# Kernel optimization log

Measured on AMD Instinct MI355X. Metric: run time of the kernel, lower is better.

## Reference

```python
import jax, jax.numpy as jnp
import numpy as np

N = 128          # seed length cfg.n
EXTRA_RANDOM = 1 # cfg.extra_random_masks


def _make_masks(n: int, extra: int) -> np.ndarray:
    i = np.arange(n, dtype=np.int64)
    # Thue-Morse: parity of popcount(i)
    tm = np.array([bin(v).count('1') & 1 for v in i], dtype=np.uint8)
    # Sierpinski: row (n-1) of Pascal's triangle mod 2 (Lucas' theorem)
    sp = (((n - 1) & i) == i).astype(np.uint8)
    masks = [sp, tm]
    rng = np.random.default_rng(1234)
    for _ in range(extra):
        masks.append(rng.integers(0, 2, size=n, dtype=np.uint8))
    return np.stack(masks, axis=0)  # (K, n)


def setup_inputs() -> dict:
    key = jax.random.key(0)
    ks = jax.random.split(key, 8)
    B, n = 64, N
    T = n * (n + 1) // 2  # 8256
    H = 1024
    x = jax.random.randint(ks[0], (B, n), 0, 2, dtype=jnp.int32)
    masks = jnp.asarray(_make_masks(n, EXTRA_RANDOM))
    def lin(k, fan_in, fan_out):
        lim = 1.0 / np.sqrt(fan_in)
        return jax.random.uniform(k, (fan_in, fan_out), jnp.float32, -lim, lim)
    W0 = lin(ks[1], T, H); b0 = jnp.zeros((H,), jnp.float32)
    W1 = lin(ks[2], H, H); b1 = jnp.zeros((H,), jnp.float32)
    Wo = lin(ks[3], H, 1); bo = jnp.zeros((1,), jnp.float32)
    return {"x": x, "masks": masks, "W0": W0, "b0": b0,
            "W1": W1, "b1": b1, "Wo": Wo, "bo": bo}


def _features(x, masks):
    # x: (B, n) ints in {0,1}; masks: (K, n) uint8
    xb = x.astype(jnp.uint8)
    B, n = xb.shape
    # L3: dihedral orbit = n rotations + n rotations of the reversal -> 2n seeds
    idx = (jnp.arange(n)[:, None] + jnp.arange(n)[None, :]) % n  # (n, n)
    rot = xb[:, idx]                # (B, n, n)
    rev = xb[:, ::-1][:, idx]       # (B, n, n)
    seeds = jnp.concatenate([rot, rev], axis=1)  # (B, 2n, n)
    # L4: keep each seed plus XOR with each mask -> (1+K) variants per seed
    masked = jnp.bitwise_xor(seeds[:, :, None, :], masks[None, None, :, :])  # (B,2n,K,n)
    all_seeds = jnp.concatenate([seeds[:, :, None, :], masked], axis=2)
    M = all_seeds.shape[1] * all_seeds.shape[2]
    all_seeds = all_seeds.reshape(B, M, n)  # (B, M, n) uint8
    # XNOR triangle: row0 = seed, row_{k+1}[j] = xnor(row_k[j], row_k[j+1])
    rows = [all_seeds]
    cur = all_seeds
    for _ in range(n - 1):
        cur = 1 - jnp.bitwise_xor(cur[..., :-1], cur[..., 1:])
        rows.append(cur)
    feats = jnp.concatenate(rows, axis=-1)          # (B, M, T(n)) uint8
    f = jnp.mean(feats, axis=1, dtype=jnp.float32)  # mean pool over transforms
    return 2.0 * f - 1.0                            # {0,1} -> {-1,+1}


def reference(x, masks, W0, b0, W1, b1, Wo, bo):
    f = _features(x, masks)
    h = jax.nn.relu(f @ W0 + b0)
    h = jax.nn.relu(h @ W1 + b1)
    return h @ Wo + bo  # (B, 1) logits
```

## Files before the change

### kernel.cpp

```cpp
#include <hip/hip_runtime.h>
#include <cstdint>

#define DEVFN __device__ __forceinline__

struct U128 { unsigned long long lo, hi; };

DEVFN U128 rotr128(U128 w, int s) {
    U128 r;
    if (s == 64) { r.lo = w.hi; r.hi = w.lo; return r; }
    if (s < 64) {
        r.lo = (w.lo >> s) | (w.hi << (64 - s));
        r.hi = (w.hi >> s) | (w.lo << (64 - s));
    } else {
        int t = s - 64;
        unsigned long long lo = w.hi, hi = w.lo;
        r.lo = (lo >> t) | (hi << (64 - t));
        r.hi = (hi >> t) | (lo << (64 - t));
    }
    return r;
}

DEVFN U128 shr128(U128 w, int s) {
    U128 r;
    if (s == 64) { r.lo = w.hi; r.hi = 0ull; return r; }
    if (s < 64) {
        r.lo = (w.lo >> s) | (w.hi << (64 - s));
        r.hi = w.hi >> s;
    } else {
        r.lo = w.hi >> (s - 64); r.hi = 0ull;
    }
    return r;
}

__global__ __launch_bounds__(256) void kB(const int* __restrict__ x,
                                          const int* __restrict__ masks,
                                          const float* __restrict__ W0,
                                          float* __restrict__ S,
                                          float* __restrict__ A2,
                                          float* __restrict__ G2) {
    int bid = blockIdx.x;
    int tid = threadIdx.x;

    if (bid == 768) {
        int b = tid >> 2;
        int rc = tid & 3;
        const int* xb = x + b * 128;
        U128 w; w.lo = 0ull; w.hi = 0ull;
        #pragma unroll
        for (int p = 0; p < 64; ++p) w.lo |= (unsigned long long)(xb[p] & 1) << p;
        #pragma unroll
        for (int p = 0; p < 64; ++p) w.hi |= (unsigned long long)(xb[64 + p] & 1) << p;
        int r0 = rc * 32;
        if (r0 & 32) { U128 t = rotr128(w, 32); w.lo ^= t.lo; w.hi ^= t.hi; }
        if (r0 & 64) { U128 t = rotr128(w, 64); w.lo ^= t.lo; w.hi ^= t.hi; }
        for (int rr = 0; rr < 32; ++rr) {
            int r = r0 + rr;
            int pc = __popcll(w.lo) + __popcll(w.hi);
            int sv = (r == 0) ? pc : (128 - pc);
            S[b * 128 + r] = (float)(2 * sv);
            U128 t = rotr128(w, 1);
            w.lo ^= t.lo; w.hi ^= t.hi;
        }
        return;
    }

    int hc = bid & 3;
    int y  = bid >> 2;
    int r, jstart, jend, slice;
    if (y < 128) { r = y >> 1; slice = y & 1; jstart = slice * 64; jend = (slice == 0) ? 64 : (128 - r); }
    else         { r = y - 64;  slice = 0;    jstart = 0;          jend = 128 - r; }
    int L = jend - jstart;

    int lane = tid & 63;
    int g    = tid >> 6;

    __shared__ unsigned long long mw[3][2];
    __shared__ float cA[64], cG[64];
    __shared__ float4 partA[4][64];
    __shared__ float4 partG[4][64];

    if (tid < 128) {
        int half = tid >> 6;
        int lane_ = tid & 63;
        #pragma unroll
        for (int k = 0; k < 3; ++k) {
            unsigned long long bal = __ballot(masks[k * 128 + half * 64 + lane_] & 1);
            if (lane_ == 0) mw[k][half] = bal;
        }
    }
    __syncthreads();
    if (tid < 64) {
        int j = jstart + tid;
        int c = 0;
        #pragma unroll
        for (int k = 0; k < 3; ++k) {
            U128 m; m.lo = mw[k][0]; m.hi = mw[k][1];
            #pragma unroll
            for (int s = 1; s <= 64; s <<= 1) {
                if (r & s) { U128 t = shr128(m, s); m.lo ^= t.lo; m.hi ^= t.hi; }
            }
            int bit = (j < 64) ? (int)((m.lo >> j) & 1) : (int)((m.hi >> (j - 64)) & 1);
            c += bit;
        }
        cA[tid] = 0.5f * (float)c - 1.0f;
        cG[tid] = (float)(2 - c) * (1.0f / 256.0f);
    }
    __syncthreads();

    int off = r * 128 - (r * (r - 1)) / 2;
    const float* base = W0 + (size_t)(off + jstart) * 1024 + hc * 256 + lane * 4;
    float4 aA = {0.f, 0.f, 0.f, 0.f}, aG = {0.f, 0.f, 0.f, 0.f};
    #pragma unroll 4
    for (int jj = g; jj < L; jj += 4) {
        float4 v = *(const float4*)(base + (size_t)jj * 1024);
        float ca = cA[jj], cg = cG[jj];
        aA.x += ca * v.x; aA.y += ca * v.y; aA.z += ca * v.z; aA.w += ca * v.w;
        aG.x += cg * v.x; aG.y += cg * v.y; aG.z += cg * v.z; aG.w += cg * v.w;
    }
    partA[g][lane] = aA;
    partG[g][lane] = aG;
    __syncthreads();

    if (tid < 64) {
        float4 sA = partA[0][tid], sG = partG[0][tid];
        #pragma unroll
        for (int gg = 1; gg < 4; ++gg) {
            float4 pA = partA[gg][tid], pG = partG[gg][tid];
            sA.x += pA.x; sA.y += pA.y; sA.z += pA.z; sA.w += pA.w;
            sG.x += pG.x; sG.y += pG.y; sG.z += pG.z; sG.w += pG.w;
        }
        int row = slice * 128 + r;
        *(float4*)(A2 + (size_t)row * 1024 + hc * 256 + tid * 4) = sA;
        *(float4*)(G2 + (size_t)row * 1024 + hc * 256 + tid * 4) = sG;
    }
}

__global__ __launch_bounds__(256) void kF(const float* __restrict__ A2,
                                          const float* __restrict__ G2,
                                          const float* __restrict__ S,
                                          const float* __restrict__ b0,
                                          const float* __restrict__ W1,
                                          float* __restrict__ z1part) {
    int hc = blockIdx.x;
    int kc = blockIdx.y;
    int bs = blockIdx.z;
    int tid = threadIdx.x;

    __shared__ float W1sh[64][128];
    __shared__ float Ssh[16][128];
    __shared__ float h0sh[16][64];

    #pragma unroll
    for (int t = 0; t < 32; ++t) {
        int idx = tid + t * 256;
        int kk = idx >> 7, hcl = idx & 127;
        W1sh[kk][hcl] = W1[(kc * 64 + kk) * 1024 + hc * 128 + hcl];
    }
    #pragma unroll
    for (int t = 0; t < 8; ++t) {
        int idx = tid + t * 256;
        int bl = idx >> 7, r = idx & 127;
        Ssh[bl][r] = S[(bs * 16 + bl) * 128 + r];
    }
    __syncthreads();

    {
        int k = tid & 63;
        int bg = tid >> 6;
        const float* a2p = A2 + kc * 64 + k;
        const float* g2p = G2 + kc * 64 + k;
        float accA = 0.f;
        float acc[4] = {0.f, 0.f, 0.f, 0.f};
        #pragma unroll 8
        for (int row = 0; row < 192; ++row) {
            float a = a2p[row * 1024];
            float g = g2p[row * 1024];
            accA += a;
            int r = row & 127;
            #pragma unroll
            for (int bb = 0; bb < 4; ++bb)
                acc[bb] += Ssh[bg * 4 + bb][r] * g;
        }
        float base = b0[kc * 64 + k] + accA;
        #pragma unroll
        for (int bb = 0; bb < 4; ++bb)
            h0sh[bg * 4 + bb][k] = fmaxf(base + acc[bb], 0.f);
    }
    __syncthreads();

    {
        int hcol = tid & 127;
        int bg2 = tid >> 7;
        float acc2[8];
        #pragma unroll
        for (int i = 0; i < 8; ++i) acc2[i] = 0.f;
        #pragma unroll 4
        for (int kk = 0; kk < 64; ++kk) {
            float w = W1sh[kk][hcol];
            #pragma unroll
            for (int bb = 0; bb < 8; ++bb)
                acc2[bb] += h0sh[bg2 * 8 + bb][kk] * w;
        }
        #pragma unroll
        for (int bb = 0; bb < 8; ++bb) {
            int b = bs * 16 + bg2 * 8 + bb;
            z1part[(kc * 64 + b) * 1024 + hc * 128 + hcol] = acc2[bb];
        }
    }
}

__global__ __launch_bounds__(1024) void kE(const float* __restrict__ z1part,
                                           const float* __restrict__ b1,
                                           const float* __restrict__ Wo,
                                           const float* __restrict__ bo,
                                           float* __restrict__ out) {
    int b = blockIdx.x;
    int h = threadIdx.x;
    float z = b1[h];
    #pragma unroll
    for (int kc = 0; kc < 16; ++kc) z += z1part[(kc * 64 + b) * 1024 + h];
    float acc = fmaxf(z, 0.f) * Wo[h];
    #pragma unroll
    for (int off = 32; off >= 1; off >>= 1) acc += __shfl_down(acc, off);
    __shared__ float red[16];
    if ((h & 63) == 0) red[h >> 6] = acc;
    __syncthreads();
    if (h == 0) {
        float s = bo[0];
        #pragma unroll
        for (int i = 0; i < 16; ++i) s += red[i];
        out[b] = s;
    }
}

extern "C" void kernel_launch(void* const* d_in, const int* in_sizes, int n_in,
                              void* d_out, int out_size, void* d_ws, size_t ws_size,
                              hipStream_t stream) {
    const int*   x     = (const int*)d_in[0];
    const int*   masks = (const int*)d_in[1];
    const float* W0    = (const float*)d_in[2];
    const float* b0    = (const float*)d_in[3];
    const float* W1    = (const float*)d_in[4];
    const float* b1    = (const float*)d_in[5];
    const float* Wo    = (const float*)d_in[6];
    const float* bo    = (const float*)d_in[7];
    float* out = (float*)d_out;

    char* ws = (char*)d_ws;
    float* S      = (float*)(ws);
    float* A2     = (float*)(ws + (32u   << 10));
    float* G2     = (float*)(ws + (800u  << 10));
    float* z1part = (float*)(ws + (1568u << 10));

    kB<<<769, 256, 0, stream>>>(x, masks, W0, S, A2, G2);
    kF<<<dim3(8, 16, 4), 256, 0, stream>>>(A2, G2, S, b0, W1, z1part);
    kE<<<64, 1024, 0, stream>>>(z1part, b1, Wo, bo, out);
}
```

Before: 36.21 us.

## Fuse final reduction kernel into kF via last-block atomic counters

Removes the separate kE launch by having the last block per (hc, bs) group, detected with an atomic counter, reduce the 16 z1part partial slices, apply bias, ReLU and the Wo dot for its columns. A second counter level picks the last hc block per batch slice to sum the per-column-chunk partials into the output. Counters are zeroed in kB's extra block. This saves one kernel launch and its gap, at the cost of threadfences, atomics and a serialized tail done by a few blocks.

```diff
diff --git a/kernel.cpp b/kernel.cpp
--- a/kernel.cpp
+++ b/kernel.cpp
@@ -37,11 +37,13 @@
                                           const float* __restrict__ W0,
                                           float* __restrict__ S,
                                           float* __restrict__ A2,
-                                          float* __restrict__ G2) {
+                                          float* __restrict__ G2,
+                                          int* __restrict__ cnt) {
     int bid = blockIdx.x;
     int tid = threadIdx.x;
 
     if (bid == 768) {
+        if (tid < 36) cnt[tid] = 0;
         int b = tid >> 2;
         int rc = tid & 3;
         const int* xb = x + b * 128;
@@ -135,12 +137,18 @@
     }
 }
 
-__global__ __launch_bounds__(256) void kF(const float* __restrict__ A2,
-                                          const float* __restrict__ G2,
-                                          const float* __restrict__ S,
-                                          const float* __restrict__ b0,
-                                          const float* __restrict__ W1,
-                                          float* __restrict__ z1part) {
+__global__ __launch_bounds__(256) void kFE(const float* __restrict__ A2,
+                                           const float* __restrict__ G2,
+                                           const float* __restrict__ S,
+                                           const float* __restrict__ b0,
+                                           const float* __restrict__ W1,
+                                           const float* __restrict__ b1,
+                                           const float* __restrict__ Wo,
+                                           const float* __restrict__ bo,
+                                           float* __restrict__ z1part,
+                                           float* __restrict__ outpart,
+                                           int* __restrict__ cnt,
+                                           float* __restrict__ out) {
     int hc = blockIdx.x;
     int kc = blockIdx.y;
     int bs = blockIdx.z;
@@ -149,6 +157,8 @@
     __shared__ float W1sh[64][128];
     __shared__ float Ssh[16][128];
     __shared__ float h0sh[16][64];
+    __shared__ float wred[2][2][8];
+    __shared__ int bc1, bc2;
 
     #pragma unroll
     for (int t = 0; t < 32; ++t) {
@@ -207,28 +217,59 @@
             z1part[(kc * 64 + b) * 1024 + hc * 128 + hcol] = acc2[bb];
         }
     }
-}
-
-__global__ __launch_bounds__(1024) void kE(const float* __restrict__ z1part,
-                                           const float* __restrict__ b1,
-                                           const float* __restrict__ Wo,
-                                           const float* __restrict__ bo,
-                                           float* __restrict__ out) {
-    int b = blockIdx.x;
-    int h = threadIdx.x;
-    float z = b1[h];
-    #pragma unroll
-    for (int kc = 0; kc < 16; ++kc) z += z1part[(kc * 64 + b) * 1024 + h];
-    float acc = fmaxf(z, 0.f) * Wo[h];
-    #pragma unroll
-    for (int off = 32; off >= 1; off >>= 1) acc += __shfl_down(acc, off);
-    __shared__ float red[16];
-    if ((h & 63) == 0) red[h >> 6] = acc;
-    __syncthreads();
-    if (h == 0) {
+    __syncthreads();
+
+    if (tid == 0) {
+        __threadfence();
+        int old = atomicAdd(&cnt[hc * 4 + bs], 1);
+        bc1 = (old == 15);
+        if (bc1) __threadfence();
+    }
+    __syncthreads();
+    if (!bc1) return;
+
+    {
+        int h = tid & 127;
+        int half = tid >> 7;
+        int hglob = hc * 128 + h;
+        float wo = Wo[hglob];
+        float bb1 = b1[hglob];
+        int wv = (tid >> 6) & 1;
+        #pragma unroll
+        for (int bl = 0; bl < 8; ++bl) {
+            int b = bs * 16 + half * 8 + bl;
+            float z = bb1;
+            #pragma unroll
+            for (int kc2 = 0; kc2 < 16; ++kc2)
+                z += z1part[(kc2 * 64 + b) * 1024 + hglob];
+            float v = fmaxf(z, 0.f) * wo;
+            #pragma unroll
+            for (int offv = 32; offv >= 1; offv >>= 1) v += __shfl_down(v, offv);
+            if ((tid & 63) == 0) wred[half][wv][bl] = v;
+        }
+    }
+    __syncthreads();
+    if (tid < 16) {
+        int half2 = tid >> 3, bl2 = tid & 7;
+        outpart[hc * 64 + bs * 16 + half2 * 8 + bl2] =
+            wred[half2][0][bl2] + wred[half2][1][bl2];
+    }
+    __syncthreads();
+
+    if (tid == 0) {
+        __threadfence();
+        int old2 = atomicAdd(&cnt[32 + bs], 1);
+        bc2 = (old2 == 7);
+        if (bc2) __threadfence();
+    }
+    __syncthreads();
+    if (!bc2) return;
+
+    if (tid < 16) {
+        int b = bs * 16 + tid;
         float s = bo[0];
         #pragma unroll
-        for (int i = 0; i < 16; ++i) s += red[i];
+        for (int hc2 = 0; hc2 < 8; ++hc2) s += outpart[hc2 * 64 + b];
         out[b] = s;
     }
 }
@@ -247,12 +288,14 @@
     float* out = (float*)d_out;
 
     char* ws = (char*)d_ws;
-    float* S      = (float*)(ws);
-    float* A2     = (float*)(ws + (32u   << 10));
-    float* G2     = (float*)(ws + (800u  << 10));
-    float* z1part = (float*)(ws + (1568u << 10));
-
-    kB<<<769, 256, 0, stream>>>(x, masks, W0, S, A2, G2);
-    kF<<<dim3(8, 16, 4), 256, 0, stream>>>(A2, G2, S, b0, W1, z1part);
-    kE<<<64, 1024, 0, stream>>>(z1part, b1, Wo, bo, out);
-}
+    float* S       = (float*)(ws);
+    float* A2      = (float*)(ws + (32u   << 10));
+    float* G2      = (float*)(ws + (800u  << 10));
+    float* z1part  = (float*)(ws + (1568u << 10));
+    float* outpart = (float*)(ws + (5664u << 10));
+    int*   cnt     = (int*)  (ws + (5666u << 10));
+
+    kB<<<769, 256, 0, stream>>>(x, masks, W0, S, A2, G2, cnt);
+    kFE<<<dim3(8, 16, 4), 256, 0, stream>>>(A2, G2, S, b0, W1, b1, Wo, bo,
+                                            z1part, outpart, cnt, out);
+}
```

Result: slower. 55.63 us (+53.6%).
